# Performance work log

Hardware: AMD Instinct MI355X
Metric: run time of the kernel (lower is better)

The kernel has to match this reference:

```python
import jax, jax.numpy as jnp
import numpy as np
import math

N_QUBITS = 14
STATE = 2 ** N_QUBITS  # 16384
BATCH = 512

# binary_matrix(n)[i, j] == bit (n-1-i) of j  (row-major reshape of [2]*n cube)
_BITS = ((jnp.arange(STATE)[None, :] >> (N_QUBITS - 1 - jnp.arange(N_QUBITS))[:, None]) & 1).astype(jnp.float32)  # [n, 2**n]


def setup_inputs() -> dict:
    key = jax.random.key(0)
    k1, k2, k3 = jax.random.split(key, 3)
    phi_real = jax.random.normal(k1, (BATCH, STATE), dtype=jnp.float32)
    phi_imag = jax.random.normal(k2, (BATCH, STATE), dtype=jnp.float32)
    thetas = jax.random.normal(k3, (BATCH, N_QUBITS), dtype=jnp.float32)
    return {"phi_real": phi_real, "phi_imag": phi_imag, "thetas": thetas}


def _fwht(x):
    """Fast Walsh-Hadamard transform over last dim (butterfly, same math as had_big).
    Order of the per-qubit butterflies is irrelevant for the full transform."""
    B, N = x.shape
    h = 1
    while h < N:
        xr = x.reshape(B, N // (2 * h), 2, h)
        a, b = xr[:, :, 0, :], xr[:, :, 1, :]
        x = jnp.stack([a + b, a - b], axis=2).reshape(B, N)
        h *= 2
    n = int(math.log2(N))
    return x * jnp.asarray(2.0 ** (-n / 2), dtype=jnp.float32)


def reference(phi_real, phi_imag, thetas):
    phi = phi_real + 1j * phi_imag  # complex64 state [B, 2**n]
    # RZ eigenvalues: exp(-i * (thetas @ binary_mask) / 2), first (only) chunk
    phase = thetas @ _BITS  # [B, 2**n]
    ev = jnp.exp(-0.5j * phase.astype(jnp.complex64))
    phi = _fwht(phi)
    phi = phi * ev
    phi = _fwht(phi)
    return phi
```

## Files before the change

### kernel.cpp

```cpp
#include <hip/hip_runtime.h>
#include <stdint.h>

#define NQ 14
#define STATE 16384
#define BATCH 512
#define THREADS 512
#define PER 32
#define STRIDE 132
#define LDS_WORDS (128 * STRIDE)
#define SCALE 6.103515625e-05f

typedef float v2f __attribute__((ext_vector_type(2)));
typedef float v4f __attribute__((ext_vector_type(4)));

__device__ __forceinline__ int adr(int row, int col) { return row * STRIDE + col; }

__device__ __forceinline__ uint32_t pkc(v2f v) {
    uint32_t w;
    asm("v_cvt_pk_bf16_f32 %0, %1, %2" : "=v"(w) : "v"(v[0]), "v"(v[1]));
    return w;
}
__device__ __forceinline__ v2f upkc(uint32_t w) {
    v2f v;
    v[0] = __uint_as_float(w << 16);
    v[1] = __uint_as_float(w & 0xFFFF0000u);
    return v;
}

template <int MAXM>
__device__ __forceinline__ void fwht_pk(v2f (&x)[PER]) {
#pragma unroll
    for (int m = 1; m <= MAXM; m <<= 1) {
#pragma unroll
        for (int r = 0; r < PER; ++r) {
            if (!(r & m)) {
                v2f a = x[r], b = x[r | m];
                x[r] = a + b;
                x[r | m] = a - b;
            }
        }
    }
}
template <int MAXM>
__device__ __forceinline__ void fwht_q(v2f (&x)[16]) {
#pragma unroll
    for (int m = 1; m <= MAXM; m <<= 1) {
#pragma unroll
        for (int u = 0; u < 16; ++u) {
            if (!(u & m)) {
                v2f a = x[u], c = x[u | m];
                x[u] = a + c;
                x[u | m] = a - c;
            }
        }
    }
}
__device__ __forceinline__ void hbf(v2f (&x)[16]) {
#pragma unroll
    for (int u = 0; u < 16; ++u) {
        float a = x[u][0], c = x[u][1];
        x[u][0] = a + c;
        x[u][1] = a - c;
    }
}


__global__ void __launch_bounds__(THREADS, 4)
rx_kernel(const float* __restrict__ phr, const float* __restrict__ phim,
          const float* __restrict__ th, float* __restrict__ out,
          long long out_limit) {
    extern __shared__ float lds[];
    uint32_t* ldsw = (uint32_t*)lds;
    const int b = blockIdx.x;
    const int t = threadIdx.x;
    v2f x[PER];

    const float* pr = phr + (size_t)b * STATE;
    const float* pi = phim + (size_t)b * STATE;
#pragma unroll
    for (int i = 0; i < 8; ++i) {
        float4 a = *(const float4*)(pr + i * 2048 + t * 4);
        float4 c = *(const float4*)(pi + i * 2048 + t * 4);
        x[4 * i]     = v2f{a.x, c.x};
        x[4 * i + 1] = v2f{a.y, c.y};
        x[4 * i + 2] = v2f{a.z, c.z};
        x[4 * i + 3] = v2f{a.w, c.w};
    }
    float w[NQ];
#pragma unroll
    for (int k = 0; k < NQ; ++k) w[k] = th[b * NQ + 13 - k];

    fwht_pk<16>(x);

    {
#pragma unroll
        for (int i = 0; i < 8; ++i) {
            uint4 v = make_uint4(pkc(x[4 * i]), pkc(x[4 * i + 1]),
                                 pkc(x[4 * i + 2]), pkc(x[4 * i + 3]));
            *(uint4*)&ldsw[adr(i * 16 + (t >> 5), (t & 31) * 4)] = v;
        }
        __syncthreads();
        const int base = adr(t >> 2, t & 3);
#pragma unroll
        for (int r = 0; r < PER; ++r) x[r] = upkc(ldsw[base + r * 4]);
    }

    fwht_pk<16>(x);

    {
        const int base = adr(t >> 2, t & 3);
#pragma unroll
        for (int r = 0; r < PER; ++r) ldsw[base + r * 4] = pkc(x[r]);
        const int base2 = adr((t >> 6) * 16, ((t >> 2) & 15) * 4 + (t & 3));
#pragma unroll
        for (int r = 0; r < PER; ++r)
            x[r] = upkc(ldsw[base2 + (r & 15) * STRIDE + (r >> 4) * 64]);
    }

    fwht_pk<8>(x);

    float tp = 0.f;
    if (t & 1)   tp += w[0];
    if (t & 2)   tp += w[1];
    if (t & 4)   tp += w[2];
    if (t & 8)   tp += w[3];
    if (t & 16)  tp += w[4];
    if (t & 32)  tp += w[5];
    if (t & 64)  tp += w[11];
    if (t & 128) tp += w[12];
    if (t & 256) tp += w[13];
    const float cd = __cosf(0.5f * w[7]);
    const float sd = __sinf(0.5f * w[7]);
    v2f q[16];
#pragma unroll
    for (int u = 0; u < 16; ++u) {
        float ph = tp;
        if (u & 1) ph += w[8];
        if (u & 2) ph += w[9];
        if (u & 4) ph += w[10];
        if (u & 8) ph += w[6];
        const float ang = -0.5f * ph;
        const float c0 = __cosf(ang) * SCALE;
        const float s0 = __sinf(ang) * SCALE;
        const float c1 = c0 * cd + s0 * sd;
        const float s1 = s0 * cd - c0 * sd;
        v2f xa = x[2 * u], xb = x[2 * u + 1];
        q[u][0] = xa[0] * c0 - xa[1] * s0;
        q[u][1] = xb[0] * c1 - xb[1] * s1;
    }

    hbf(q);
    fwht_q<4>(q);

    {
        const int base2 = adr((t >> 6) * 16, ((t >> 2) & 15) * 4 + (t & 3));
#pragma unroll
        for (int u = 0; u < 16; ++u) {
            lds[base2 + ((2 * u) & 15) * STRIDE + (u >> 3) * 64]     = q[u][0];
            lds[base2 + ((2 * u + 1) & 15) * STRIDE + (u >> 3) * 64] = q[u][1];
        }
        const int base = adr(t >> 2, t & 3);
#pragma unroll
        for (int u = 0; u < 16; ++u)
            q[u] = v2f{lds[base + 8 * u], lds[base + 8 * u + 4]};
    }

    hbf(q);
    fwht_q<8>(q);

    {
        const int base = adr(t >> 2, t & 3);
#pragma unroll
        for (int u = 0; u < 16; ++u) {
            lds[base + 8 * u]     = q[u][0];
            lds[base + 8 * u + 4] = q[u][1];
        }
        __syncthreads();
#pragma unroll
        for (int i = 0; i < 8; ++i) {
            float4 v = *(const float4*)&lds[adr(i * 16 + (t >> 5), (t & 31) * 4)];
            q[2 * i]     = v2f{v.x, v.y};
            q[2 * i + 1] = v2f{v.z, v.w};
        }
    }

    hbf(q);
    fwht_q<8>(q);

    float* o = out + (size_t)b * STATE;
    const long long ob = (long long)b * STATE;
#pragma unroll
    for (int i = 0; i < 8; ++i) {
        const int s0 = i * 2048 + t * 4;
        if (ob + s0 + 3 < out_limit) {
            v4f vv = {q[2 * i][0], q[2 * i][1], q[2 * i + 1][0], q[2 * i + 1][1]};
            __builtin_nontemporal_store(vv, (v4f*)(o + s0));
        }
    }
}

extern "C" void kernel_launch(void* const* d_in, const int* in_sizes, int n_in,
                              void* d_out, int out_size, void* d_ws, size_t ws_size,
                              hipStream_t stream) {
    const float* phr  = (const float*)d_in[0];
    const float* phim = (const float*)d_in[1];
    const float* th   = (const float*)d_in[2];
    float* out = (float*)d_out;
    (void)hipFuncSetAttribute((const void*)rx_kernel,
                              hipFuncAttributeMaxDynamicSharedMemorySize,
                              LDS_WORDS * (int)sizeof(float));
    rx_kernel<<<BATCH, THREADS, LDS_WORDS * sizeof(float), stream>>>(
        phr, phim, th, out, (long long)out_size);
}
```

Measured before the change: 107.1 us.

## Process two batch rows per block, prefetching the second row during the first

The grid is halved to 256 blocks and each block handles two batch rows. The second row is loaded into registers up front so its global load latency overlaps the first row's transform. __syncthreads is replaced by an inline-asm lgkmcnt wait plus s_barrier, which avoids waiting on outstanding global loads. Holding a second 32-element register array doubles register pressure, and launch bounds drop to 2 blocks per SM, which lowers occupancy and may cause spills.

After: 112.0 us. +4.6%, slower.

```diff
diff --git a/kernel.cpp b/kernel.cpp
--- a/kernel.cpp
+++ b/kernel.cpp
@@ -4,6 +4,7 @@
 #define NQ 14
 #define STATE 16384
 #define BATCH 512
+#define GRID 256
 #define THREADS 512
 #define PER 32
 #define STRIDE 132
@@ -12,6 +13,8 @@
 
 typedef float v2f __attribute__((ext_vector_type(2)));
 typedef float v4f __attribute__((ext_vector_type(4)));
+
+#define BAR() asm volatile("s_waitcnt lgkmcnt(0)\n\ts_barrier" ::: "memory")
 
 __device__ __forceinline__ int adr(int row, int col) { return row * STRIDE + col; }
 
@@ -65,18 +68,11 @@
 }
 
 
-__global__ void __launch_bounds__(THREADS, 4)
-rx_kernel(const float* __restrict__ phr, const float* __restrict__ phim,
-          const float* __restrict__ th, float* __restrict__ out,
-          long long out_limit) {
-    extern __shared__ float lds[];
-    uint32_t* ldsw = (uint32_t*)lds;
-    const int b = blockIdx.x;
-    const int t = threadIdx.x;
-    v2f x[PER];
-
-    const float* pr = phr + (size_t)b * STATE;
-    const float* pi = phim + (size_t)b * STATE;
+__device__ __forceinline__ void load_row(const float* __restrict__ phr,
+                                         const float* __restrict__ phim,
+                                         int row, int t, v2f (&x)[PER]) {
+    const float* pr = phr + (size_t)row * STATE;
+    const float* pi = phim + (size_t)row * STATE;
 #pragma unroll
     for (int i = 0; i < 8; ++i) {
         float4 a = *(const float4*)(pr + i * 2048 + t * 4);
@@ -86,10 +82,12 @@
         x[4 * i + 2] = v2f{a.z, c.z};
         x[4 * i + 3] = v2f{a.w, c.w};
     }
-    float w[NQ];
-#pragma unroll
-    for (int k = 0; k < NQ; ++k) w[k] = th[b * NQ + 13 - k];
-
+}
+
+__device__ __forceinline__ void process_row(v2f (&x)[PER], const float (&w)[NQ],
+                                            float* lds, uint32_t* ldsw, int t,
+                                            float* o, long long ob,
+                                            long long out_limit) {
     fwht_pk<16>(x);
 
     {
@@ -99,7 +97,7 @@
                                  pkc(x[4 * i + 2]), pkc(x[4 * i + 3]));
             *(uint4*)&ldsw[adr(i * 16 + (t >> 5), (t & 31) * 4)] = v;
         }
-        __syncthreads();
+        BAR();
         const int base = adr(t >> 2, t & 3);
 #pragma unroll
         for (int r = 0; r < PER; ++r) x[r] = upkc(ldsw[base + r * 4]);
@@ -175,7 +173,7 @@
             lds[base + 8 * u]     = q[u][0];
             lds[base + 8 * u + 4] = q[u][1];
         }
-        __syncthreads();
+        BAR();
 #pragma unroll
         for (int i = 0; i < 8; ++i) {
             float4 v = *(const float4*)&lds[adr(i * 16 + (t >> 5), (t & 31) * 4)];
@@ -187,8 +185,6 @@
     hbf(q);
     fwht_q<8>(q);
 
-    float* o = out + (size_t)b * STATE;
-    const long long ob = (long long)b * STATE;
 #pragma unroll
     for (int i = 0; i < 8; ++i) {
         const int s0 = i * 2048 + t * 4;
@@ -197,6 +193,36 @@
             __builtin_nontemporal_store(vv, (v4f*)(o + s0));
         }
     }
+}
+
+__global__ void __launch_bounds__(THREADS, 2)
+rx_kernel(const float* __restrict__ phr, const float* __restrict__ phim,
+          const float* __restrict__ th, float* __restrict__ out,
+          long long out_limit) {
+    extern __shared__ float lds[];
+    uint32_t* ldsw = (uint32_t*)lds;
+    const int b = blockIdx.x;
+    const int t = threadIdx.x;
+    const int rA = b, rB = b + GRID;
+
+    v2f x[PER], y[PER];
+    load_row(phr, phim, rA, t, x);
+    load_row(phr, phim, rB, t, y);
+    float wA[NQ];
+#pragma unroll
+    for (int k = 0; k < NQ; ++k) wA[k] = th[rA * NQ + 13 - k];
+
+    process_row(x, wA, lds, ldsw, t, out + (size_t)rA * STATE,
+                (long long)rA * STATE, out_limit);
+
+    float wB[NQ];
+#pragma unroll
+    for (int k = 0; k < NQ; ++k) wB[k] = th[rB * NQ + 13 - k];
+
+    BAR();
+
+    process_row(y, wB, lds, ldsw, t, out + (size_t)rB * STATE,
+                (long long)rB * STATE, out_limit);
 }
 
 extern "C" void kernel_launch(void* const* d_in, const int* in_sizes, int n_in,
@@ -209,6 +235,6 @@
     (void)hipFuncSetAttribute((const void*)rx_kernel,
                               hipFuncAttributeMaxDynamicSharedMemorySize,
                               LDS_WORDS * (int)sizeof(float));
-    rx_kernel<<<BATCH, THREADS, LDS_WORDS * sizeof(float), stream>>>(
+    rx_kernel<<<GRID, THREADS, LDS_WORDS * sizeof(float), stream>>>(
         phr, phim, th, out, (long long)out_size);
 }
```
